# Kernel tuning notes

Measured on AMD Instinct MI355X. Metric: run time of the kernel, lower is better.

Reference implementation:

```python
import jax, jax.numpy as jnp
import numpy as np

D_MODEL = 1024
H = 16
D_K = D_MODEL // H
D_FF = 4096
EPS = 1e-6


def layer_norm(x, alpha, bias):
    mean = jnp.mean(x, axis=-1, keepdims=True)
    var = jnp.mean((x - mean) ** 2, axis=-1, keepdims=True)  # unbiased=False
    return alpha * (x - mean) / jnp.sqrt(var + EPS) + bias


def setup_inputs() -> dict:
    key = jax.random.key(0)
    ks = jax.random.split(key, 8)
    B, S = 4, 2048
    sd = 1.0 / np.sqrt(D_MODEL)
    x = jax.random.normal(ks[0], (B, S, D_MODEL), dtype=jnp.float32)
    src_mask = jnp.ones((B, 1, S), dtype=jnp.int32)
    wq = jax.random.normal(ks[1], (D_MODEL, D_MODEL), jnp.float32) * sd
    wk = jax.random.normal(ks[2], (D_MODEL, D_MODEL), jnp.float32) * sd
    wv = jax.random.normal(ks[3], (D_MODEL, D_MODEL), jnp.float32) * sd
    wo = jax.random.normal(ks[4], (D_MODEL, D_MODEL), jnp.float32) * sd
    w1 = jax.random.normal(ks[5], (D_FF, D_MODEL), jnp.float32) * sd
    b1 = jnp.zeros((D_FF,), jnp.float32)
    w2 = jax.random.normal(ks[6], (D_MODEL, D_FF), jnp.float32) * (1.0 / np.sqrt(D_FF))
    b2 = jnp.zeros((D_MODEL,), jnp.float32)
    ln1_a = jnp.ones((D_MODEL,), jnp.float32)
    ln1_b = jnp.zeros((D_MODEL,), jnp.float32)
    ln2_a = jnp.ones((D_MODEL,), jnp.float32)
    ln2_b = jnp.zeros((D_MODEL,), jnp.float32)
    return dict(x=x, src_mask=src_mask, wq=wq, wk=wk, wv=wv, wo=wo,
                ln1_a=ln1_a, ln1_b=ln1_b, ln2_a=ln2_a, ln2_b=ln2_b,
                w1=w1, b1=b1, w2=w2, b2=b2)


def attention(xn, wq, wk, wv, wo, src_mask):
    B, S, _ = xn.shape
    # torch nn.Linear: y = x @ W.T
    q = (xn @ wq.T).reshape(B, S, H, D_K).transpose(0, 2, 1, 3)  # [B,H,S,Dk]
    k = (xn @ wk.T).reshape(B, S, H, D_K).transpose(0, 2, 1, 3)
    v = (xn @ wv.T).reshape(B, S, H, D_K).transpose(0, 2, 1, 3)
    scores = jnp.einsum('bhqd,bhkd->bhqk', q, k) / np.sqrt(D_K)
    m = src_mask[:, None, :, :]  # [B,1,1,S] from [B,1,S]
    scores = jnp.where(m == 0, -jnp.inf, scores)
    attn = jax.nn.softmax(scores, axis=-1)
    out = jnp.einsum('bhqk,bhkd->bhqd', attn, v)
    out = out.transpose(0, 2, 1, 3).reshape(B, S, D_MODEL)
    return out @ wo.T


def reference(x, src_mask, wq, wk, wv, wo, ln1_a, ln1_b, ln2_a, ln2_b, w1, b1, w2, b2):
    # pre-LN residual 1: self-attention
    xn = layer_norm(x, ln1_a, ln1_b)
    x = x + attention(xn, wq, wk, wv, wo, src_mask)
    # pre-LN residual 2: FFN
    xn = layer_norm(x, ln2_a, ln2_b)
    h = jax.nn.relu(xn @ w1.T + b1)
    x = x + (h @ w2.T + b2)
    return x
```

## Files before the change

### kernel.cpp

```cpp
#include <hip/hip_runtime.h>
#include <stdint.h>

typedef unsigned short u16;
typedef __bf16 bf16x8 __attribute__((ext_vector_type(8)));
typedef float   f32x4 __attribute__((ext_vector_type(4)));
typedef u16     u16x8 __attribute__((ext_vector_type(8)));
typedef u16     u16x4 __attribute__((ext_vector_type(4)));

__device__ __forceinline__ u16 f2bf(float f) {
    union { float f; uint32_t i; } c; c.f = f;
    uint32_t r = c.i + 0x7FFFu + ((c.i >> 16) & 1u);
    return (u16)(r >> 16);
}
__device__ __forceinline__ uint32_t cvt_pk_bf16(float lo, float hi) {
    uint32_t r;
    asm("v_cvt_pk_bf16_f32 %0, %1, %2" : "=v"(r) : "v"(lo), "v"(hi));
    return r;
}
__device__ __forceinline__ void gload_lds16(const u16* g, u16* l) {
    __builtin_amdgcn_global_load_lds(
        (__attribute__((address_space(1))) void*)(g),
        (__attribute__((address_space(3))) void*)(l), 16, 0, 0);
}

__global__ __launch_bounds__(256) void cvt_all(
    const float* __restrict__ wq, const float* __restrict__ wk,
    const float* __restrict__ wv, const float* __restrict__ wo,
    const float* __restrict__ w1, const float* __restrict__ w2,
    u16* __restrict__ wqb, u16* __restrict__ wkb, u16* __restrict__ wvb,
    u16* __restrict__ wob, u16* __restrict__ w1b, u16* __restrict__ w2b)
{
    int blk = blockIdx.x;
    const float* src; u16* dst; int off;
    if      (blk < 1024)  { src = wq; dst = wqb; off = blk; }
    else if (blk < 2048)  { src = wk; dst = wkb; off = blk - 1024; }
    else if (blk < 3072)  { src = wv; dst = wvb; off = blk - 2048; }
    else if (blk < 4096)  { src = wo; dst = wob; off = blk - 3072; }
    else if (blk < 8192)  { src = w1; dst = w1b; off = blk - 4096; }
    else                  { src = w2; dst = w2b; off = blk - 8192; }
    int i = off * 1024 + threadIdx.x * 4;
    float4 v = *(const float4*)(src + i);
    u16x4 o; o[0] = f2bf(v.x); o[1] = f2bf(v.y); o[2] = f2bf(v.z); o[3] = f2bf(v.w);
    *(u16x4*)(dst + i) = o;
}

__global__ __launch_bounds__(256) void ln_kernel(
    const float* __restrict__ x, const float* __restrict__ ga,
    const float* __restrict__ be, u16* __restrict__ out)
{
    const int D = 1024;
    int row  = blockIdx.x * 4 + (threadIdx.x >> 6);
    int lane = threadIdx.x & 63;
    const float* xr = x + (size_t)row * D + lane * 16;
    float f[16];
#pragma unroll
    for (int i = 0; i < 4; ++i) *(float4*)&f[i * 4] = *(const float4*)(xr + i * 4);
    float s = 0.f, s2 = 0.f;
#pragma unroll
    for (int i = 0; i < 16; ++i) { s += f[i]; s2 += f[i] * f[i]; }
#pragma unroll
    for (int off = 1; off < 64; off <<= 1) {
        s  += __shfl_xor(s,  off, 64);
        s2 += __shfl_xor(s2, off, 64);
    }
    float mean = s * (1.0f / 1024.0f);
    float var  = s2 * (1.0f / 1024.0f) - mean * mean;
    var = var < 0.f ? 0.f : var;
    float inv = 1.0f / sqrtf(var + 1e-6f);
    float g[16], b[16];
#pragma unroll
    for (int i = 0; i < 4; ++i) {
        *(float4*)&g[i * 4] = *(const float4*)(ga + lane * 16 + i * 4);
        *(float4*)&b[i * 4] = *(const float4*)(be + lane * 16 + i * 4);
    }
    u16x8 o0, o1;
#pragma unroll
    for (int i = 0; i < 8; ++i) {
        o0[i] = f2bf(g[i]     * (f[i]     - mean) * inv + b[i]);
        o1[i] = f2bf(g[8 + i] * (f[8 + i] - mean) * inv + b[8 + i]);
    }
    u16* orow = out + (size_t)row * D + lane * 16;
    *(u16x8*)(orow)     = o0;
    *(u16x8*)(orow + 8) = o1;
}

__device__ __forceinline__ void gemm256_core(
    const u16* __restrict__ A, const u16* __restrict__ W,
    int K, int ldw, int row_a0, int row_w0,
    u16* smem, f32x4 (&acc)[4][4])
{
    int tid  = threadIdx.x;
    int lane = tid & 63;
    int quad = lane >> 4, l16 = lane & 15;
    int wave = tid >> 6;
    int wm = wave >> 2, wn = wave & 3;

    const u16* as0 = A + (size_t)(row_a0 + (tid >> 2)) * K   + (tid & 3) * 8;
    const u16* bs0 = W + (size_t)(row_w0 + (tid >> 2)) * ldw + (tid & 3) * 8;
    const u16* bs1 = bs0 + (size_t)128 * ldw;
    u16* d_a0 = smem + tid * 8;
    u16* d_a1 = smem + 4096  + tid * 8;
    u16* d_b00 = smem + 8192  + tid * 8;
    u16* d_b01 = smem + 12288 + tid * 8;
    u16* d_b10 = smem + 16384 + tid * 8;
    u16* d_b11 = smem + 20480 + tid * 8;

    const int nk = K >> 6;
    gload_lds16(as0,      d_a0);
    gload_lds16(as0 + 32, d_a1);
    gload_lds16(bs0,      d_b00);
    gload_lds16(bs0 + 32, d_b10);
    gload_lds16(bs1,      d_b01);
    gload_lds16(bs1 + 32, d_b11);
    __syncthreads();

    const int aoff = (wm * 64 + l16) * 32 + quad * 8;
    const int boff = (wn * 64 + l16) * 32 + quad * 8;

    for (int t = 0; t < nk; ++t) {
        const int cb = (t & 1) * 24576;
        if (t + 1 < nk) {
            const int nb = ((t + 1) & 1) * 24576;
            const int k0 = (t + 1) * 64;
            gload_lds16(as0 + k0,      d_a0  + nb);
            gload_lds16(as0 + k0 + 32, d_a1  + nb);
            gload_lds16(bs0 + k0,      d_b00 + nb);
            gload_lds16(bs0 + k0 + 32, d_b10 + nb);
            gload_lds16(bs1 + k0,      d_b01 + nb);
            gload_lds16(bs1 + k0 + 32, d_b11 + nb);
        }
#pragma unroll
        for (int h = 0; h < 2; ++h) {
            const u16* Ah = smem + cb + h * 4096;
            const u16* Bh = smem + cb + 8192 + h * 8192;
            bf16x8 af[4], bf[4];
#pragma unroll
            for (int mt = 0; mt < 4; ++mt)
                af[mt] = *(const bf16x8*)(&Ah[aoff + mt * 512]);
#pragma unroll
            for (int nt = 0; nt < 4; ++nt)
                bf[nt] = *(const bf16x8*)(&Bh[boff + nt * 512]);
#pragma unroll
            for (int mt = 0; mt < 4; ++mt)
#pragma unroll
                for (int nt = 0; nt < 4; ++nt)
                    acc[mt][nt] = __builtin_amdgcn_mfma_f32_16x16x32_bf16(
                        af[mt], bf[nt], acc[mt][nt], 0, 0, 0);
        }
        __syncthreads();
    }
}

template<bool OUTF32>
__global__ __launch_bounds__(512, 2) void gemm256(
    const u16* __restrict__ A, const u16* __restrict__ W,
    const float* __restrict__ bias, const float* __restrict__ resid,
    void* __restrict__ Cp, int M, int N, int K, int ldw, int do_relu)
{
    __shared__ u16 smem[49152];
    int tid  = threadIdx.x;
    int lane = tid & 63, wave = tid >> 6;
    int quad = lane >> 4, l16 = lane & 15;
    int wm = wave >> 2, wn = wave & 3;
    const int row_a0 = blockIdx.x * 128, row_w0 = blockIdx.y * 256;
    f32x4 acc[4][4] = {};
    gemm256_core(A, W, K, ldw, row_a0, row_w0, smem, acc);
#pragma unroll
    for (int mt = 0; mt < 4; ++mt) {
#pragma unroll
        for (int nt = 0; nt < 4; ++nt) {
#pragma unroll
            for (int r = 0; r < 4; ++r) {
                int grow = row_a0 + wm * 64 + mt * 16 + quad * 4 + r;
                int gcol = row_w0 + wn * 64 + nt * 16 + l16;
                float vv = acc[mt][nt][r];
                if (bias)    vv += bias[gcol];
                if (do_relu) vv = vv > 0.f ? vv : 0.f;
                if (resid)   vv += resid[(size_t)grow * N + gcol];
                if (OUTF32) ((float*)Cp)[(size_t)grow * N + gcol] = vv;
                else        ((u16*)Cp)[(size_t)grow * N + gcol] = f2bf(vv);
            }
        }
    }
}

__device__ __forceinline__ void gemm256sq_core(
    const u16* __restrict__ A, const u16* __restrict__ W,
    int K, int ldw, int row_a0, int row_w0,
    u16* smem, f32x4 (&acc)[8][4])
{
    int tid  = threadIdx.x;
    int lane = tid & 63;
    int quad = lane >> 4, l16 = lane & 15;
    int wave = tid >> 6;
    int wm = wave >> 2, wn = wave & 3;

    int srow = tid >> 2, scol = (tid & 3) * 8;
    const u16* a0 = A + (size_t)(row_a0 + srow) * K + scol;
    const u16* a1 = A + (size_t)(row_a0 + 128 + srow) * K + scol;
    const u16* b0 = W + (size_t)(row_w0 + srow) * ldw + scol;
    const u16* b1 = W + (size_t)(row_w0 + 128 + srow) * ldw + scol;
    u16* dst = smem + tid * 8;
    const int nk = K >> 6;

    gload_lds16(a0,      dst);
    gload_lds16(a1,      dst + 4096);
    gload_lds16(a0 + 32, dst + 8192);
    gload_lds16(a1 + 32, dst + 12288);
    gload_lds16(b0,      dst + 16384);
    gload_lds16(b1,      dst + 20480);
    gload_lds16(b0 + 32, dst + 24576);
    gload_lds16(b1 + 32, dst + 28672);
    __syncthreads();

    const int abase = wm * 4096 + l16 * 32 + quad * 8;
    const int bbase = 16384 + (wn >> 1) * 4096 + ((wn & 1) * 64 + l16) * 32 + quad * 8;

    for (int t = 0; t < nk; ++t) {
        const int cb = (t & 1) << 15;
        if (t + 1 < nk) {
            const int nb = ((t + 1) & 1) << 15;
            const int k0 = (t + 1) * 64;
            u16* nd = dst + nb;
            gload_lds16(a0 + k0,      nd);
            gload_lds16(a1 + k0,      nd + 4096);
            gload_lds16(a0 + k0 + 32, nd + 8192);
            gload_lds16(a1 + k0 + 32, nd + 12288);
            gload_lds16(b0 + k0,      nd + 16384);
            gload_lds16(b1 + k0,      nd + 20480);
            gload_lds16(b0 + k0 + 32, nd + 24576);
            gload_lds16(b1 + k0 + 32, nd + 28672);
        }
#pragma unroll
        for (int h = 0; h < 2; ++h) {
            const u16* base = smem + cb + h * 8192;
            bf16x8 af[8], bf[4];
#pragma unroll
            for (int mt = 0; mt < 8; ++mt)
                af[mt] = *(const bf16x8*)(&base[abase + mt * 512]);
#pragma unroll
            for (int nt = 0; nt < 4; ++nt)
                bf[nt] = *(const bf16x8*)(&base[bbase + nt * 512]);
#pragma unroll
            for (int mt = 0; mt < 8; ++mt)
#pragma unroll
                for (int nt = 0; nt < 4; ++nt)
                    acc[mt][nt] = __builtin_amdgcn_mfma_f32_16x16x32_bf16(
                        af[mt], bf[nt], acc[mt][nt], 0, 0, 0);
        }
        __syncthreads();
    }
}

template<bool OUTF32>
__global__ __launch_bounds__(512, 2) void gemm256sq(
    const u16* __restrict__ A, const u16* __restrict__ W,
    const float* __restrict__ bias, const float* __restrict__ resid,
    void* __restrict__ Cp, int M, int N, int K, int ldw, int do_relu)
{
    __shared__ u16 smem[65536];
    int tid  = threadIdx.x;
    int lane = tid & 63, wave = tid >> 6;
    int quad = lane >> 4, l16 = lane & 15;
    int wm = wave >> 2, wn = wave & 3;
    const int row_a0 = blockIdx.x * 256, row_w0 = blockIdx.y * 256;
    f32x4 acc[8][4] = {};
    gemm256sq_core(A, W, K, ldw, row_a0, row_w0, smem, acc);
#pragma unroll
    for (int mt = 0; mt < 8; ++mt) {
#pragma unroll
        for (int nt = 0; nt < 4; ++nt) {
#pragma unroll
            for (int r = 0; r < 4; ++r) {
                int grow = row_a0 + wm * 128 + mt * 16 + quad * 4 + r;
                int gcol = row_w0 + wn * 64 + nt * 16 + l16;
                float vv = acc[mt][nt][r];
                if (bias)    vv += bias[gcol];
                if (do_relu) vv = vv > 0.f ? vv : 0.f;
                if (resid)   vv += resid[(size_t)grow * N + gcol];
                if (OUTF32) ((float*)Cp)[(size_t)grow * N + gcol] = vv;
                else        ((u16*)Cp)[(size_t)grow * N + gcol] = f2bf(vv);
            }
        }
    }
}

__global__ __launch_bounds__(512, 2) void gemm256sq_qkv(
    const u16* __restrict__ A, const u16* __restrict__ Wqkv,
    u16* __restrict__ qo, u16* __restrict__ ko, u16* __restrict__ vo, int K)
{
    __shared__ u16 smem[65536];
    int tid  = threadIdx.x;
    int lane = tid & 63, wave = tid >> 6;
    int quad = lane >> 4, l16 = lane & 15;
    int wm = wave >> 2, wn = wave & 3;
    const int row_a0 = blockIdx.x * 256, row_w0 = blockIdx.y * 256;
    f32x4 acc[8][4] = {};
    gemm256sq_core(A, Wqkv, K, K, row_a0, row_w0, smem, acc);
    int seg = row_w0 >> 10;
    u16* dst = (seg == 0) ? qo : (seg == 1) ? ko : vo;
    int col0 = row_w0 & 1023;
#pragma unroll
    for (int mt = 0; mt < 8; ++mt) {
#pragma unroll
        for (int nt = 0; nt < 4; ++nt) {
#pragma unroll
            for (int r = 0; r < 4; ++r) {
                int grow = row_a0 + wm * 128 + mt * 16 + quad * 4 + r;
                int gcol = col0 + wn * 64 + nt * 16 + l16;
                dst[(size_t)grow * 1024 + gcol] = f2bf(acc[mt][nt][r]);
            }
        }
    }
}

__global__ __launch_bounds__(512, 4) void attn_kernel(
    const u16* __restrict__ Q, const u16* __restrict__ Km, const u16* __restrict__ Vm,
    const int* __restrict__ mask, u16* __restrict__ O)
{
    const int S = 2048, DM = 1024;
    const float C1 = 0.18033688f;
    const float C0 = -11.541560f;
    __shared__ u16 smem[35840];
    u16* Ks0 = smem;
    u16* Ks1 = smem + 4096;
    u16* Vt0 = smem + 8192;
    u16* Vt1 = smem + 12800;
    u16* Ps  = smem + 17408;
    u16* Qs  = smem + 17408;

    int qt = blockIdx.x, bh = blockIdx.y;
    int b = bh >> 4, h = bh & 15;
    int tid = threadIdx.x;
    int wave = tid >> 6, lane = tid & 63;
    int quad = lane >> 4, l16 = lane & 15;
    size_t base = (size_t)b * S;
    size_t hoff = (size_t)h * 64;

    {
        int r = tid >> 1, c0 = (tid & 1) * 32;
        const u16* src = Q + (base + qt * 256 + r) * DM + hoff + c0;
        u16* dq = Qs + r * 72 + c0;
        *(u16x8*)(dq)      = *(const u16x8*)(src);
        *(u16x8*)(dq + 8)  = *(const u16x8*)(src + 8);
        *(u16x8*)(dq + 16) = *(const u16x8*)(src + 16);
        *(u16x8*)(dq + 24) = *(const u16x8*)(src + 24);
    }
    const u16* ksrc = Km + (base + (tid >> 3)) * DM + hoff
                    + ((tid & 7) ^ ((tid >> 5) & 7)) * 8;
    int kp = tid & 31, d0 = (tid >> 5) * 4;
    const u16* vsrc = Vm + (base + kp * 2) * DM + hoff + d0;
    const int* msrc = mask + b * S + 4 * l16;

    __syncthreads();
    const int q0 = wave * 32;
    bf16x8 qf00 = *(const bf16x8*)(&Qs[(q0 + l16) * 72 + quad * 8]);
    bf16x8 qf01 = *(const bf16x8*)(&Qs[(q0 + l16) * 72 + 32 + quad * 8]);
    bf16x8 qf10 = *(const bf16x8*)(&Qs[(q0 + 16 + l16) * 72 + quad * 8]);
    bf16x8 qf11 = *(const bf16x8*)(&Qs[(q0 + 16 + l16) * 72 + 32 + quad * 8]);
    const int swz = (l16 & 7) * 8;
    const int u0  = (quad * 8) ^ swz;

    {
        u16x4 va = *(const u16x4*)(vsrc);
        u16x4 vb = *(const u16x4*)(vsrc + DM);
        gload_lds16(ksrc, Ks0 + tid * 8);
        ksrc += 64 * DM; vsrc += 64 * DM;
#pragma unroll
        for (int i = 0; i < 4; ++i) {
            uint32_t w = (uint32_t)va[i] | ((uint32_t)vb[i] << 16);
            *(uint32_t*)(&Vt0[(d0 + i) * 72 + kp * 2]) = w;
        }
    }
    __syncthreads();

    float l0[4] = {0.f, 0.f, 0.f, 0.f};
    float l1[4] = {0.f, 0.f, 0.f, 0.f};
    f32x4 o0[4] = {}, o1[4] = {};

    for (int it = 0; it < 32; ++it) {
        const u16* Kcur = (it & 1) ? Ks1 : Ks0;
        const u16* Vcur = (it & 1) ? Vt1 : Vt0;
        u16* Knxt = (it & 1) ? Ks0 : Ks1;
        u16* Vnxt = (it & 1) ? Vt0 : Vt1;
        const bool pfch = (it < 31);
        u16x4 va, vb;
        if (pfch) {
            va = *(const u16x4*)(vsrc);
            vb = *(const u16x4*)(vsrc + DM);
            gload_lds16(ksrc, Knxt + tid * 8);
            ksrc += 64 * DM; vsrc += 64 * DM;
        }
        f32x4 s0[4] = {}, s1[4] = {};
#pragma unroll
        for (int t = 0; t < 4; ++t) {
            const u16* krp = Kcur + (4 * l16 + t) * 64;
            bf16x8 kf0 = *(const bf16x8*)(krp + u0);
            bf16x8 kf1 = *(const bf16x8*)(krp + (u0 ^ 32));
            s0[t] = __builtin_amdgcn_mfma_f32_16x16x32_bf16(qf00, kf0, s0[t], 0, 0, 0);
            s0[t] = __builtin_amdgcn_mfma_f32_16x16x32_bf16(qf01, kf1, s0[t], 0, 0, 0);
            s1[t] = __builtin_amdgcn_mfma_f32_16x16x32_bf16(qf10, kf0, s1[t], 0, 0, 0);
            s1[t] = __builtin_amdgcn_mfma_f32_16x16x32_bf16(qf11, kf1, s1[t], 0, 0, 0);
        }
        int4 mk4 = *(const int4*)(msrc); msrc += 64;
        float c0t[4];
        c0t[0] = (mk4.x == 0) ? -1e38f : C0;
        c0t[1] = (mk4.y == 0) ? -1e38f : C0;
        c0t[2] = (mk4.z == 0) ? -1e38f : C0;
        c0t[3] = (mk4.w == 0) ? -1e38f : C0;
#pragma unroll
        for (int r = 0; r < 4; ++r) {
            float p0 = exp2f(fmaf(s0[0][r], C1, c0t[0]));
            float p1 = exp2f(fmaf(s0[1][r], C1, c0t[1]));
            float p2 = exp2f(fmaf(s0[2][r], C1, c0t[2]));
            float p3 = exp2f(fmaf(s0[3][r], C1, c0t[3]));
            l0[r] += (p0 + p1) + (p2 + p3);
            uint2 pw;
            pw.x = cvt_pk_bf16(p0, p1);
            pw.y = cvt_pk_bf16(p2, p3);
            *(uint2*)(&Ps[(q0 + quad * 4 + r) * 72 + 4 * l16]) = pw;
        }
#pragma unroll
        for (int r = 0; r < 4; ++r) {
            float p0 = exp2f(fmaf(s1[0][r], C1, c0t[0]));
            float p1 = exp2f(fmaf(s1[1][r], C1, c0t[1]));
            float p2 = exp2f(fmaf(s1[2][r], C1, c0t[2]));
            float p3 = exp2f(fmaf(s1[3][r], C1, c0t[3]));
            l1[r] += (p0 + p1) + (p2 + p3);
            uint2 pw;
            pw.x = cvt_pk_bf16(p0, p1);
            pw.y = cvt_pk_bf16(p2, p3);
            *(uint2*)(&Ps[(q0 + 16 + quad * 4 + r) * 72 + 4 * l16]) = pw;
        }
        bf16x8 pf00 = *(const bf16x8*)(&Ps[(q0 + l16) * 72 + quad * 8]);
        bf16x8 pf01 = *(const bf16x8*)(&Ps[(q0 + l16) * 72 + 32 + quad * 8]);
        bf16x8 pf10 = *(const bf16x8*)(&Ps[(q0 + 16 + l16) * 72 + quad * 8]);
        bf16x8 pf11 = *(const bf16x8*)(&Ps[(q0 + 16 + l16) * 72 + 32 + quad * 8]);
#pragma unroll
        for (int t = 0; t < 4; ++t) {
            bf16x8 vf0 = *(const bf16x8*)(&Vcur[(t * 16 + l16) * 72 + quad * 8]);
            bf16x8 vf1 = *(const bf16x8*)(&Vcur[(t * 16 + l16) * 72 + 32 + quad * 8]);
            o0[t] = __builtin_amdgcn_mfma_f32_16x16x32_bf16(pf00, vf0, o0[t], 0, 0, 0);
            o0[t] = __builtin_amdgcn_mfma_f32_16x16x32_bf16(pf01, vf1, o0[t], 0, 0, 0);
            o1[t] = __builtin_amdgcn_mfma_f32_16x16x32_bf16(pf10, vf0, o1[t], 0, 0, 0);
            o1[t] = __builtin_amdgcn_mfma_f32_16x16x32_bf16(pf11, vf1, o1[t], 0, 0, 0);
        }
        if (pfch) {
#pragma unroll
            for (int i = 0; i < 4; ++i) {
                uint32_t w = (uint32_t)va[i] | ((uint32_t)vb[i] << 16);
                *(uint32_t*)(&Vnxt[(d0 + i) * 72 + kp * 2]) = w;
            }
        }
        __syncthreads();
    }
#pragma unroll
    for (int r = 0; r < 4; ++r) {
#pragma unroll
        for (int off = 1; off < 16; off <<= 1) {
            l0[r] += __shfl_xor(l0[r], off, 16);
            l1[r] += __shfl_xor(l1[r], off, 16);
        }
        float i0 = 1.0f / l0[r];
        float i1 = 1.0f / l1[r];
        u16* dst0 = O + (base + qt * 256 + q0 + quad * 4 + r) * DM + hoff + l16;
        u16* dst1 = dst0 + (size_t)16 * DM;
#pragma unroll
        for (int t = 0; t < 4; ++t) {
            dst0[t * 16] = f2bf(o0[t][r] * i0);
            dst1[t * 16] = f2bf(o1[t][r] * i1);
        }
    }
}

extern "C" void kernel_launch(void* const* d_in, const int* in_sizes, int n_in,
                              void* d_out, int out_size, void* d_ws, size_t ws_size,
                              hipStream_t stream)
{
    (void)in_sizes; (void)n_in; (void)out_size; (void)ws_size;
    const float* x    = (const float*)d_in[0];
    const int*   mask = (const int*)d_in[1];
    const float* wq   = (const float*)d_in[2];
    const float* wk   = (const float*)d_in[3];
    const float* wv   = (const float*)d_in[4];
    const float* wo   = (const float*)d_in[5];
    const float* ln1a = (const float*)d_in[6];
    const float* ln1b = (const float*)d_in[7];
    const float* ln2a = (const float*)d_in[8];
    const float* ln2b = (const float*)d_in[9];
    const float* w1   = (const float*)d_in[10];
    const float* b1   = (const float*)d_in[11];
    const float* w2   = (const float*)d_in[12];
    const float* b2   = (const float*)d_in[13];

    const int M = 8192, D = 1024, F = 4096;
    char* ws = (char*)d_ws;
    u16*  wqkv = (u16*)(ws);
    u16*  wqb = wqkv;
    u16*  wkb = (u16*)(ws + (2u  << 20));
    u16*  wvb = (u16*)(ws + (4u  << 20));
    u16*  wob = (u16*)(ws + (6u  << 20));
    u16*  w1b = (u16*)(ws + (8u  << 20));
    u16*  w2b = (u16*)(ws + (16u << 20));
    u16*  xn  = (u16*)(ws + (24u << 20));
    u16*  q   = (u16*)(ws + (40u << 20));
    u16*  hb  = (u16*)(ws + (40u << 20));

    u16*   kbuf = (u16*)d_out;
    u16*   vbuf = (u16*)d_out + (size_t)M * D;
    float* x1   = (float*)d_out;

    cvt_all<<<12288, 256, 0, stream>>>(wq, wk, wv, wo, w1, w2,
                                       wqb, wkb, wvb, wob, w1b, w2b);

    ln_kernel<<<M / 4, 256, 0, stream>>>(x, ln1a, ln1b, xn);
    dim3 gq(M / 256, 3072 / 256);
    gemm256sq_qkv<<<gq, 512, 0, stream>>>(xn, wqkv, q, kbuf, vbuf, D);
    dim3 ga(2048 / 256, 64);
    attn_kernel<<<ga, 512, 0, stream>>>(q, kbuf, vbuf, mask, xn);
    dim3 g1(M / 128, D / 256);
    gemm256<true ><<<g1, 512, 0, stream>>>(xn, wob, nullptr, x, x1, M, D, D, D, 0);
    ln_kernel<<<M / 4, 256, 0, stream>>>(x1, ln2a, ln2b, xn);
    dim3 gf1(M / 256, 2048 / 256);
    dim3 gf2(M / 128, D / 256);
    gemm256sq<false><<<gf1, 512, 0, stream>>>(xn, w1b, b1, nullptr, hb, M, 2048, D, D, 1);
    gemm256<true ><<<gf2, 512, 0, stream>>>(hb, w2b, nullptr, x1, x1, M, D, 2048, F, 0);
    gemm256sq<false><<<gf1, 512, 0, stream>>>(xn, w1b + (size_t)2048 * D, b1 + 2048, nullptr, hb, M, 2048, D, D, 1);
    gemm256<true ><<<gf2, 512, 0, stream>>>(hb, w2b + 2048, b2, x1, x1, M, D, 2048, F, 0);
}
```

Before: 587.6 us.

## Replace double-buffered GEMM mainloops with 4-stage LDS ring and vmcnt waits

Rewrites both GEMM core loops to use a four-slot LDS ring with 32-wide K steps, prefetching three stages ahead. The full __syncthreads after each step becomes a partial s_waitcnt vmcnt plus s_barrier, so later loads stay in flight while the current stage is computed. The goal is to hide global-load latency and cut the stall at each barrier. In exchange the loop runs twice as many iterations, each with half the work and its own barrier, and correctness now rests on manual vmcnt counting.

```diff
diff --git a/kernel.cpp b/kernel.cpp
--- a/kernel.cpp
+++ b/kernel.cpp
@@ -21,6 +21,10 @@
     __builtin_amdgcn_global_load_lds(
         (__attribute__((address_space(1))) void*)(g),
         (__attribute__((address_space(3))) void*)(l), 16, 0, 0);
+}
+template<int N>
+__device__ __forceinline__ void wait_vm_barrier() {
+    asm volatile("s_waitcnt vmcnt(%0)\n\ts_barrier" :: "n"(N) : "memory");
 }
 
 __global__ __launch_bounds__(256) void cvt_all(
@@ -84,10 +88,11 @@
     *(u16x8*)(orow + 8) = o1;
 }
 
-__device__ __forceinline__ void gemm256_core(
+
+__device__ __forceinline__ void gemm_ring256_core(
     const u16* __restrict__ A, const u16* __restrict__ W,
     int K, int ldw, int row_a0, int row_w0,
-    u16* smem, f32x4 (&acc)[4][4])
+    u16* smem, f32x4 (&acc)[8][4])
 {
     int tid  = threadIdx.x;
     int lane = tid & 63;
@@ -95,99 +100,61 @@
     int wave = tid >> 6;
     int wm = wave >> 2, wn = wave & 3;
 
-    const u16* as0 = A + (size_t)(row_a0 + (tid >> 2)) * K   + (tid & 3) * 8;
-    const u16* bs0 = W + (size_t)(row_w0 + (tid >> 2)) * ldw + (tid & 3) * 8;
-    const u16* bs1 = bs0 + (size_t)128 * ldw;
-    u16* d_a0 = smem + tid * 8;
-    u16* d_a1 = smem + 4096  + tid * 8;
-    u16* d_b00 = smem + 8192  + tid * 8;
-    u16* d_b01 = smem + 12288 + tid * 8;
-    u16* d_b10 = smem + 16384 + tid * 8;
-    u16* d_b11 = smem + 20480 + tid * 8;
-
-    const int nk = K >> 6;
-    gload_lds16(as0,      d_a0);
-    gload_lds16(as0 + 32, d_a1);
-    gload_lds16(bs0,      d_b00);
-    gload_lds16(bs0 + 32, d_b10);
-    gload_lds16(bs1,      d_b01);
-    gload_lds16(bs1 + 32, d_b11);
-    __syncthreads();
-
-    const int aoff = (wm * 64 + l16) * 32 + quad * 8;
-    const int boff = (wn * 64 + l16) * 32 + quad * 8;
+    int srow = tid >> 2, scol = (tid & 3) * 8;
+    const u16* a0 = A + (size_t)(row_a0 + srow) * K + scol;
+    const u16* a1 = a0 + (size_t)128 * K;
+    const u16* b0 = W + (size_t)(row_w0 + srow) * ldw + scol;
+    const u16* b1 = b0 + (size_t)128 * ldw;
+    u16* dst = smem + tid * 8;
+    const int nk = K >> 5;
+
+#pragma unroll
+    for (int s = 0; s < 3; ++s) {
+        u16* d = dst + s * 16384;
+        const int k = s * 32;
+        gload_lds16(a0 + k, d);
+        gload_lds16(a1 + k, d + 4096);
+        gload_lds16(b0 + k, d + 8192);
+        gload_lds16(b1 + k, d + 12288);
+    }
+    const int abase = wm * 4096 + l16 * 32 + quad * 8;
+    const int bbase = 8192 + (wn >> 1) * 4096 + ((wn & 1) * 64 + l16) * 32 + quad * 8;
+
+    wait_vm_barrier<8>();
 
     for (int t = 0; t < nk; ++t) {
-        const int cb = (t & 1) * 24576;
-        if (t + 1 < nk) {
-            const int nb = ((t + 1) & 1) * 24576;
-            const int k0 = (t + 1) * 64;
-            gload_lds16(as0 + k0,      d_a0  + nb);
-            gload_lds16(as0 + k0 + 32, d_a1  + nb);
-            gload_lds16(bs0 + k0,      d_b00 + nb);
-            gload_lds16(bs0 + k0 + 32, d_b10 + nb);
-            gload_lds16(bs1 + k0,      d_b01 + nb);
-            gload_lds16(bs1 + k0 + 32, d_b11 + nb);
-        }
-#pragma unroll
-        for (int h = 0; h < 2; ++h) {
-            const u16* Ah = smem + cb + h * 4096;
-            const u16* Bh = smem + cb + 8192 + h * 8192;
-            bf16x8 af[4], bf[4];
-#pragma unroll
-            for (int mt = 0; mt < 4; ++mt)
-                af[mt] = *(const bf16x8*)(&Ah[aoff + mt * 512]);
+        if (t + 3 < nk) {
+            u16* d = dst + ((t + 3) & 3) * 16384;
+            const int k = (t + 3) * 32;
+            gload_lds16(a0 + k, d);
+            gload_lds16(a1 + k, d + 4096);
+            gload_lds16(b0 + k, d + 8192);
+            gload_lds16(b1 + k, d + 12288);
+        }
+        const u16* buf = smem + (t & 3) * 16384;
+        bf16x8 af[8], bf[4];
+#pragma unroll
+        for (int mt = 0; mt < 8; ++mt)
+            af[mt] = *(const bf16x8*)(&buf[abase + mt * 512]);
+#pragma unroll
+        for (int nt = 0; nt < 4; ++nt)
+            bf[nt] = *(const bf16x8*)(&buf[bbase + nt * 512]);
+#pragma unroll
+        for (int mt = 0; mt < 8; ++mt)
 #pragma unroll
             for (int nt = 0; nt < 4; ++nt)
-                bf[nt] = *(const bf16x8*)(&Bh[boff + nt * 512]);
-#pragma unroll
-            for (int mt = 0; mt < 4; ++mt)
-#pragma unroll
-                for (int nt = 0; nt < 4; ++nt)
-                    acc[mt][nt] = __builtin_amdgcn_mfma_f32_16x16x32_bf16(
-                        af[mt], bf[nt], acc[mt][nt], 0, 0, 0);
-        }
-        __syncthreads();
-    }
-}
-
-template<bool OUTF32>
-__global__ __launch_bounds__(512, 2) void gemm256(
-    const u16* __restrict__ A, const u16* __restrict__ W,
-    const float* __restrict__ bias, const float* __restrict__ resid,
-    void* __restrict__ Cp, int M, int N, int K, int ldw, int do_relu)
-{
-    __shared__ u16 smem[49152];
-    int tid  = threadIdx.x;
-    int lane = tid & 63, wave = tid >> 6;
-    int quad = lane >> 4, l16 = lane & 15;
-    int wm = wave >> 2, wn = wave & 3;
-    const int row_a0 = blockIdx.x * 128, row_w0 = blockIdx.y * 256;
-    f32x4 acc[4][4] = {};
-    gemm256_core(A, W, K, ldw, row_a0, row_w0, smem, acc);
-#pragma unroll
-    for (int mt = 0; mt < 4; ++mt) {
-#pragma unroll
-        for (int nt = 0; nt < 4; ++nt) {
-#pragma unroll
-            for (int r = 0; r < 4; ++r) {
-                int grow = row_a0 + wm * 64 + mt * 16 + quad * 4 + r;
-                int gcol = row_w0 + wn * 64 + nt * 16 + l16;
-                float vv = acc[mt][nt][r];
-                if (bias)    vv += bias[gcol];
-                if (do_relu) vv = vv > 0.f ? vv : 0.f;
-                if (resid)   vv += resid[(size_t)grow * N + gcol];
-                if (OUTF32) ((float*)Cp)[(size_t)grow * N + gcol] = vv;
-                else        ((u16*)Cp)[(size_t)grow * N + gcol] = f2bf(vv);
-            }
-        }
-    }
-}
-
-__device__ __forceinline__ void gemm256sq_core(
+                acc[mt][nt] = __builtin_amdgcn_mfma_f32_16x16x32_bf16(
+                    af[mt], bf[nt], acc[mt][nt], 0, 0, 0);
+        if      (t + 3 < nk) wait_vm_barrier<8>();
+        else if (t + 2 < nk) wait_vm_barrier<4>();
+        else if (t + 1 < nk) wait_vm_barrier<0>();
+    }
+}
+
+__device__ __forceinline__ void gemm_ring128_core(
     const u16* __restrict__ A, const u16* __restrict__ W,
     int K, int ldw, int row_a0, int row_w0,
-    u16* smem, f32x4 (&acc)[8][4])
+    u16* smem, f32x4 (&acc)[4][4])
 {
     int tid  = threadIdx.x;
     int lane = tid & 63;
@@ -197,58 +164,49 @@
 
     int srow = tid >> 2, scol = (tid & 3) * 8;
     const u16* a0 = A + (size_t)(row_a0 + srow) * K + scol;
-    const u16* a1 = A + (size_t)(row_a0 + 128 + srow) * K + scol;
     const u16* b0 = W + (size_t)(row_w0 + srow) * ldw + scol;
-    const u16* b1 = W + (size_t)(row_w0 + 128 + srow) * ldw + scol;
+    const u16* b1 = b0 + (size_t)128 * ldw;
     u16* dst = smem + tid * 8;
-    const int nk = K >> 6;
-
-    gload_lds16(a0,      dst);
-    gload_lds16(a1,      dst + 4096);
-    gload_lds16(a0 + 32, dst + 8192);
-    gload_lds16(a1 + 32, dst + 12288);
-    gload_lds16(b0,      dst + 16384);
-    gload_lds16(b1,      dst + 20480);
-    gload_lds16(b0 + 32, dst + 24576);
-    gload_lds16(b1 + 32, dst + 28672);
-    __syncthreads();
-
-    const int abase = wm * 4096 + l16 * 32 + quad * 8;
-    const int bbase = 16384 + (wn >> 1) * 4096 + ((wn & 1) * 64 + l16) * 32 + quad * 8;
+    const int nk = K >> 5;
+
+#pragma unroll
+    for (int s = 0; s < 3; ++s) {
+        u16* d = dst + s * 12288;
+        const int k = s * 32;
+        gload_lds16(a0 + k, d);
+        gload_lds16(b0 + k, d + 4096);
+        gload_lds16(b1 + k, d + 8192);
+    }
+    const int abase = (wm * 64 + l16) * 32 + quad * 8;
+    const int bbase = 4096 + (wn >> 1) * 4096 + ((wn & 1) * 64 + l16) * 32 + quad * 8;
+
+    wait_vm_barrier<6>();
 
     for (int t = 0; t < nk; ++t) {
-        const int cb = (t & 1) << 15;
-        if (t + 1 < nk) {
-            const int nb = ((t + 1) & 1) << 15;
-            const int k0 = (t + 1) * 64;
-            u16* nd = dst + nb;
-            gload_lds16(a0 + k0,      nd);
-            gload_lds16(a1 + k0,      nd + 4096);
-            gload_lds16(a0 + k0 + 32, nd + 8192);
-            gload_lds16(a1 + k0 + 32, nd + 12288);
-            gload_lds16(b0 + k0,      nd + 16384);
-            gload_lds16(b1 + k0,      nd + 20480);
-            gload_lds16(b0 + k0 + 32, nd + 24576);
-            gload_lds16(b1 + k0 + 32, nd + 28672);
-        }
-#pragma unroll
-        for (int h = 0; h < 2; ++h) {
-            const u16* base = smem + cb + h * 8192;
-            bf16x8 af[8], bf[4];
-#pragma unroll
-            for (int mt = 0; mt < 8; ++mt)
-                af[mt] = *(const bf16x8*)(&base[abase + mt * 512]);
+        if (t + 3 < nk) {
+            u16* d = dst + ((t + 3) & 3) * 12288;
+            const int k = (t + 3) * 32;
+            gload_lds16(a0 + k, d);
+            gload_lds16(b0 + k, d + 4096);
+            gload_lds16(b1 + k, d + 8192);
+        }
+        const u16* buf = smem + (t & 3) * 12288;
+        bf16x8 af[4], bf[4];
+#pragma unroll
+        for (int mt = 0; mt < 4; ++mt)
+            af[mt] = *(const bf16x8*)(&buf[abase + mt * 512]);
+#pragma unroll
+        for (int nt = 0; nt < 4; ++nt)
+            bf[nt] = *(const bf16x8*)(&buf[bbase + nt * 512]);
+#pragma unroll
+        for (int mt = 0; mt < 4; ++mt)
 #pragma unroll
             for (int nt = 0; nt < 4; ++nt)
-                bf[nt] = *(const bf16x8*)(&base[bbase + nt * 512]);
-#pragma unroll
-            for (int mt = 0; mt < 8; ++mt)
-#pragma unroll
-                for (int nt = 0; nt < 4; ++nt)
-                    acc[mt][nt] = __builtin_amdgcn_mfma_f32_16x16x32_bf16(
-                        af[mt], bf[nt], acc[mt][nt], 0, 0, 0);
-        }
-        __syncthreads();
+                acc[mt][nt] = __builtin_amdgcn_mfma_f32_16x16x32_bf16(
+                    af[mt], bf[nt], acc[mt][nt], 0, 0, 0);
+        if      (t + 3 < nk) wait_vm_barrier<6>();
+        else if (t + 2 < nk) wait_vm_barrier<3>();
+        else if (t + 1 < nk) wait_vm_barrier<0>();
     }
 }
 
@@ -265,7 +223,7 @@
     int wm = wave >> 2, wn = wave & 3;
     const int row_a0 = blockIdx.x * 256, row_w0 = blockIdx.y * 256;
     f32x4 acc[8][4] = {};
-    gemm256sq_core(A, W, K, ldw, row_a0, row_w0, smem, acc);
+    gemm_ring256_core(A, W, K, ldw, row_a0, row_w0, smem, acc);
 #pragma unroll
     for (int mt = 0; mt < 8; ++mt) {
 #pragma unroll
@@ -296,7 +254,7 @@
     int wm = wave >> 2, wn = wave & 3;
     const int row_a0 = blockIdx.x * 256, row_w0 = blockIdx.y * 256;
     f32x4 acc[8][4] = {};
-    gemm256sq_core(A, Wqkv, K, K, row_a0, row_w0, smem, acc);
+    gemm_ring256_core(A, Wqkv, K, K, row_a0, row_w0, smem, acc);
     int seg = row_w0 >> 10;
     u16* dst = (seg == 0) ? qo : (seg == 1) ? ko : vo;
     int col0 = row_w0 & 1023;
@@ -309,6 +267,39 @@
                 int grow = row_a0 + wm * 128 + mt * 16 + quad * 4 + r;
                 int gcol = col0 + wn * 64 + nt * 16 + l16;
                 dst[(size_t)grow * 1024 + gcol] = f2bf(acc[mt][nt][r]);
+            }
+        }
+    }
+}
+
+template<bool OUTF32>
+__global__ __launch_bounds__(512, 2) void gemm128x256(
+    const u16* __restrict__ A, const u16* __restrict__ W,
+    const float* __restrict__ bias, const float* __restrict__ resid,
+    void* __restrict__ Cp, int M, int N, int K, int ldw, int do_relu)
+{
+    __shared__ u16 smem[49152];
+    int tid  = threadIdx.x;
+    int lane = tid & 63, wave = tid >> 6;
+    int quad = lane >> 4, l16 = lane & 15;
+    int wm = wave >> 2, wn = wave & 3;
+    const int row_a0 = blockIdx.x * 128, row_w0 = blockIdx.y * 256;
+    f32x4 acc[4][4] = {};
+    gemm_ring128_core(A, W, K, ldw, row_a0, row_w0, smem, acc);
+#pragma unroll
+    for (int mt = 0; mt < 4; ++mt) {
+#pragma unroll
+        for (int nt = 0; nt < 4; ++nt) {
+#pragma unroll
+            for (int r = 0; r < 4; ++r) {
+                int grow = row_a0 + wm * 64 + mt * 16 + quad * 4 + r;
+                int gcol = row_w0 + wn * 64 + nt * 16 + l16;
+                float vv = acc[mt][nt][r];
+                if (bias)    vv += bias[gcol];
+                if (do_relu) vv = vv > 0.f ? vv : 0.f;
+                if (resid)   vv += resid[(size_t)grow * N + gcol];
+                if (OUTF32) ((float*)Cp)[(size_t)grow * N + gcol] = vv;
+                else        ((u16*)Cp)[(size_t)grow * N + gcol] = f2bf(vv);
             }
         }
     }
@@ -519,12 +510,12 @@
     dim3 ga(2048 / 256, 64);
     attn_kernel<<<ga, 512, 0, stream>>>(q, kbuf, vbuf, mask, xn);
     dim3 g1(M / 128, D / 256);
-    gemm256<true ><<<g1, 512, 0, stream>>>(xn, wob, nullptr, x, x1, M, D, D, D, 0);
+    gemm128x256<true ><<<g1, 512, 0, stream>>>(xn, wob, nullptr, x, x1, M, D, D, D, 0);
     ln_kernel<<<M / 4, 256, 0, stream>>>(x1, ln2a, ln2b, xn);
     dim3 gf1(M / 256, 2048 / 256);
     dim3 gf2(M / 128, D / 256);
     gemm256sq<false><<<gf1, 512, 0, stream>>>(xn, w1b, b1, nullptr, hb, M, 2048, D, D, 1);
-    gemm256<true ><<<gf2, 512, 0, stream>>>(hb, w2b, nullptr, x1, x1, M, D, 2048, F, 0);
+    gemm128x256<true ><<<gf2, 512, 0, stream>>>(hb, w2b, nullptr, x1, x1, M, D, 2048, F, 0);
     gemm256sq<false><<<gf1, 512, 0, stream>>>(xn, w1b + (size_t)2048 * D, b1 + 2048, nullptr, hb, M, 2048, D, D, 1);
-    gemm256<true ><<<gf2, 512, 0, stream>>>(hb, w2b + 2048, b2, x1, x1, M, D, 2048, F, 0);
-}
+    gemm128x256<true ><<<gf2, 512, 0, stream>>>(hb, w2b + 2048, b2, x1, x1, M, D, 2048, F, 0);
+}
```

Result: no change. 588.3 us (+0.1%).
